# Performance work log

Hardware: AMD Instinct MI355X
Metric: run time of the kernel (lower is better)

The kernel has to match this reference:

```python
import jax, jax.numpy as jnp
import numpy as np

N_NODES = 65536
VOCAB = 1000
IN_DIM = 256
MEM_DIM = 256
HIDDEN = 256
NUM_CLASSES = 2


def _rand_parents(rng, n):
    # parent[i] < i for i >= 1 ; node 0 is the root (parent entry unused/masked)
    p = np.zeros(n, dtype=np.int64)
    p[1:] = rng.integers(0, np.arange(1, n))
    return jnp.asarray(p, dtype=jnp.int32)


def setup_inputs() -> dict:
    key = jax.random.key(0)
    ks = jax.random.split(key, 16)
    rng = np.random.default_rng(0)
    s = 0.05
    return {
        "l_tokens": jax.random.randint(ks[0], (N_NODES,), 0, VOCAB, dtype=jnp.int32),
        "l_parent": _rand_parents(rng, N_NODES),
        "r_tokens": jax.random.randint(ks[1], (N_NODES,), 0, VOCAB, dtype=jnp.int32),
        "r_parent": _rand_parents(rng, N_NODES),
        "emb_W": jax.random.normal(ks[2], (VOCAB, IN_DIM), jnp.float32) * s,
        "Wioux": jax.random.normal(ks[3], (IN_DIM, 3 * MEM_DIM), jnp.float32) * s,
        "bioux": jax.random.normal(ks[4], (3 * MEM_DIM,), jnp.float32) * s,
        "Wiouh": jax.random.normal(ks[5], (MEM_DIM, 3 * MEM_DIM), jnp.float32) * s,
        "biouh": jax.random.normal(ks[6], (3 * MEM_DIM,), jnp.float32) * s,
        "Wfx": jax.random.normal(ks[7], (IN_DIM, MEM_DIM), jnp.float32) * s,
        "bfx": jax.random.normal(ks[8], (MEM_DIM,), jnp.float32) * s,
        "Wfh": jax.random.normal(ks[9], (MEM_DIM, MEM_DIM), jnp.float32) * s,
        "bfh": jax.random.normal(ks[10], (MEM_DIM,), jnp.float32) * s,
        "Wh": jax.random.normal(ks[11], (2 * MEM_DIM, HIDDEN), jnp.float32) * s,
        "bh": jax.random.normal(ks[12], (HIDDEN,), jnp.float32) * s,
        "Wp": jax.random.normal(ks[13], (HIDDEN, NUM_CLASSES), jnp.float32) * s,
        "bp": jax.random.normal(ks[14], (NUM_CLASSES,), jnp.float32) * s,
    }


def _tree_lstm_root_c(tokens, parent, emb_W, Wioux, bioux, Wiouh, biouh,
                      Wfx, bfx, Wfh, bfh):
    # Batched x-dependent projections (faithful: ioux(emb), fx(emb))
    X = emb_W[tokens]                       # [N, in_dim]
    ioux_all = X @ Wioux + bioux            # [N, 3M]
    fx_all = X @ Wfx + bfx                  # [N, M]
    n = tokens.shape[0]
    m = Wfh.shape[0]

    def step(carry, i):
        h_sum, fc_sum, c_root = carry
        # ChildSumTreeLSTM.node_forward for node i
        iou = ioux_all[i] + h_sum[i] @ Wiouh + biouh
        ig, og, ug = jnp.split(iou, 3)
        c = jax.nn.sigmoid(ig) * jnp.tanh(ug) + fc_sum[i]   # leaf: fc_sum=0, h_sum=0
        h = jax.nn.sigmoid(og) * jnp.tanh(c)
        # forget-gate contribution of node i to its parent p:
        p = parent[i]
        f = jax.nn.sigmoid(h @ Wfh + bfh + fx_all[p])
        mask = (i != 0).astype(h.dtype)      # root has no parent
        h_sum = h_sum.at[p].add(h * mask)
        fc_sum = fc_sum.at[p].add(f * c * mask)
        c_root = jnp.where(i == 0, c, c_root)
        return (h_sum, fc_sum, c_root), None

    init = (jnp.zeros((n, m), X.dtype), jnp.zeros((n, m), X.dtype),
            jnp.zeros((m,), X.dtype))
    # children-before-parents order: descending index (parent[i] < i)
    (h_sum, fc_sum, c_root), _ = jax.lax.scan(step, init, jnp.arange(n - 1, -1, -1))
    return c_root                            # lstate == root cell state c


def reference(l_tokens, l_parent, r_tokens, r_parent, emb_W, Wioux, bioux,
              Wiouh, biouh, Wfx, bfx, Wfh, bfh, Wh, bh, Wp, bp):
    cl = _tree_lstm_root_c(l_tokens, l_parent, emb_W, Wioux, bioux, Wiouh,
                           biouh, Wfx, bfx, Wfh, bfh)
    cr = _tree_lstm_root_c(r_tokens, r_parent, emb_W, Wioux, bioux, Wiouh,
                           biouh, Wfx, bfx, Wfh, bfh)
    # Similarity head on root cell states
    vec = jnp.concatenate([cl * cr, jnp.abs(cl - cr)])[None, :]  # [1, 2M]
    hid = jax.nn.sigmoid(vec @ Wh + bh)
    return jax.nn.softmax(hid @ Wp + bp, axis=1)                 # [1, num_classes]
```

## Files before the change

### kernel.cpp

```cpp
#include <hip/hip_runtime.h>
#include <math.h>

#define NN 65536
#define TWO_N (2 * NN)
#define VOCAB 1000
#define MD 256
#define G3 768
#define DMAX 65536
#define HALF (DMAX / 2)
#define DCAP 128
#define NB 64
#define NT 256
#define NTS 1024
#define NSPAN 1024
#define SPAN 128
#define NTEAMS 64

typedef __attribute__((ext_vector_type(8))) short bf16x8;
typedef __attribute__((ext_vector_type(4))) float f32x4;

struct Params {
    const int* l_tokens; const int* l_parent;
    const int* r_tokens; const int* r_parent;
    const float* emb_W;
    const float* Wioux; const float* bioux;
    const float* Wiouh; const float* biouh;
    const float* Wfx;   const float* bfx;
    const float* Wfh;   const float* bfh;
    const float* Wh;    const float* bh;
    const float* Wp;    const float* bp;
    float* out;
    float* E_ioux;
    float* E_fx;
    float* C_leaf;
    float* H_leaf;
    float* FH_leaf;
    unsigned int* Wiouh_p;
    unsigned int* Wfh_p;
    float* h_sum;
    float* fc_sum;
    float* c_root;
    unsigned short* hstage;
    int* tarr;
    unsigned long long* ad_a;
    unsigned long long* ad_b;
    int* hc;
    int* pending;
    int* pend2;
    int* rank;
    int* lstart;
    int* blocksum;
    int* cnt; int* offs; int* cur;
    int* order;
    int* lorder;
    int* gtab;
    int* gdb;
    int* ecut;
    int* dbase;
    int* maxd;
    int cap_rows;
};

struct SWT {
    unsigned int wiou[12 * 2048];
    unsigned short hbufA[NB * MD];
    int nid[2][NB]; int row[2][NB]; int prow[2][NB];
    int tok[2][NB]; int ptok[2][NB]; int pgid[2][NB];
};

__device__ __forceinline__ float sigmoidf_(float x) {
    return 1.0f / (1.0f + __expf(-x));
}
__device__ __forceinline__ float tanhf_(float x) {
    float ex = __expf(2.0f * x);
    return 1.0f - 2.0f / (ex + 1.0f);
}
__device__ __forceinline__ unsigned int bf16rne_(float x) {
    unsigned int b = __float_as_uint(x);
    return (b + 0x7FFFu + ((b >> 16) & 1u)) >> 16;
}
__device__ __forceinline__ int aload_(int* p) {
    return __hip_atomic_load(p, __ATOMIC_RELAXED, __HIP_MEMORY_SCOPE_AGENT);
}
__device__ __forceinline__ float acohf_(const float* p) {
    return __hip_atomic_load((float*)p, __ATOMIC_RELAXED,
                             __HIP_MEMORY_SCOPE_AGENT);
}
__device__ __forceinline__ unsigned long long acohu64_(const void* p) {
    return __hip_atomic_load((unsigned long long*)p, __ATOMIC_RELAXED,
                             __HIP_MEMORY_SCOPE_AGENT);
}
__device__ __forceinline__ int dep_(const Params& P, int g) {
    return ((const int*)P.ad_a)[2 * g];
}
__device__ __forceinline__ int rowr(const Params& P, int tree, int d, int lr) {
    int r = P.dbase[tree * HALF + d] + lr;
    if (r >= P.cap_rows) r -= P.cap_rows;
    return r;
}

__global__ __launch_bounds__(NT) void k_prep(Params P) {
    __shared__ float es[4][MD];
    const int t = threadIdx.x, bid = blockIdx.x, nblk = gridDim.x;
    const int gsize = nblk * NT, gtid = bid * NT + t;
    for (int u = gtid; u < 48 * 2048; u += gsize) {
        int tl = u >> 11, rem = u & 2047;
        int kb = rem >> 8, rem2 = rem & 255;
        int ln = rem2 >> 2, jj = (rem2 & 3) << 1;
        int k = kb * 32 + (ln >> 4) * 8 + jj;
        int n = tl * 16 + (ln & 15);
        float x0 = P.Wiouh[(size_t)k * G3 + n];
        float x1 = P.Wiouh[(size_t)(k + 1) * G3 + n];
        P.Wiouh_p[u] = bf16rne_(x0) | (bf16rne_(x1) << 16);
    }
    for (int u = gtid; u < 16 * 2048; u += gsize) {
        int tl = u >> 11, rem = u & 2047;
        int kb = rem >> 8, rem2 = rem & 255;
        int ln = rem2 >> 2, jj = (rem2 & 3) << 1;
        int k = kb * 32 + (ln >> 4) * 8 + jj;
        int n = tl * 16 + (ln & 15);
        float x0 = P.Wfh[(size_t)k * MD + n];
        float x1 = P.Wfh[(size_t)(k + 1) * MD + n];
        P.Wfh_p[u] = bf16rne_(x0) | (bf16rne_(x1) << 16);
    }
    for (int v0 = bid * 4; v0 < VOCAB; v0 += nblk * 4) {
        __syncthreads();
        #pragma unroll
        for (int r = 0; r < 4; ++r)
            es[r][t] = (v0 + r < VOCAB) ? P.emb_W[(size_t)(v0 + r) * MD + t] : 0.f;
        __syncthreads();
        float a0[4] = {0.f,0.f,0.f,0.f}, a1[4] = {0.f,0.f,0.f,0.f};
        float a2[4] = {0.f,0.f,0.f,0.f}, a3[4] = {0.f,0.f,0.f,0.f};
        for (int k = 0; k < MD; ++k) {
            float wi = P.Wioux[k * G3 + t];
            float wo = P.Wioux[k * G3 + 256 + t];
            float wu = P.Wioux[k * G3 + 512 + t];
            float wf = P.Wfx[k * MD + t];
            #pragma unroll
            for (int r = 0; r < 4; ++r) {
                float e = es[r][k];
                a0[r] += wi * e; a1[r] += wo * e; a2[r] += wu * e; a3[r] += wf * e;
            }
        }
        float bi = P.bioux[t], bo = P.bioux[256 + t], bu = P.bioux[512 + t], bf = P.bfx[t];
        float hb_i = P.biouh[t], hb_o = P.biouh[256 + t], hb_u = P.biouh[512 + t];
        __syncthreads();
        for (int r = 0; r < 4; ++r) {
            float hl = 0.f;
            if (v0 + r < VOCAB) {
                float ei = a0[r] + bi, eo = a1[r] + bo, eu = a2[r] + bu;
                P.E_ioux[(size_t)(v0 + r) * G3 + t]       = ei;
                P.E_ioux[(size_t)(v0 + r) * G3 + 256 + t] = eo;
                P.E_ioux[(size_t)(v0 + r) * G3 + 512 + t] = eu;
                P.E_fx[(size_t)(v0 + r) * MD + t]         = a3[r] + bf;
                float cl = sigmoidf_(ei + hb_i) * tanhf_(eu + hb_u);
                hl = sigmoidf_(eo + hb_o) * tanhf_(cl);
                P.C_leaf[(size_t)(v0 + r) * MD + t] = cl;
                P.H_leaf[(size_t)(v0 + r) * MD + t] = hl;
            }
            es[r][t] = hl;
        }
        __syncthreads();
        float af[4] = {0.f,0.f,0.f,0.f};
        for (int k = 0; k < MD; ++k) {
            float wf = P.Wfh[(size_t)k * MD + t];
            #pragma unroll
            for (int r = 0; r < 4; ++r) af[r] += wf * es[r][k];
        }
        for (int r = 0; r < 4; ++r)
            if (v0 + r < VOCAB) P.FH_leaf[(size_t)(v0 + r) * MD + t] = af[r];
        __syncthreads();
    }
    for (int g = gtid; g < TWO_N; g += gsize) {
        int tree = g >> 16, i = g & (NN - 1);
        if (i == 0) {
            P.ad_a[g] = ((unsigned long long)g << 32);
        } else {
            const int* par = tree ? P.r_parent : P.l_parent;
            int pg = (tree << 16) | par[i];
            P.ad_a[g] = ((unsigned long long)pg << 32) | 1ull;
            P.hc[pg] = 1;
        }
    }
}

__global__ __launch_bounds__(NT) void k_double(Params P, int it) {
    const int gtid = blockIdx.x * NT + threadIdx.x;
    const int gsize = gridDim.x * NT;
    if (it == 0) {
        for (int g = gtid; g < TWO_N; g += gsize) {
            int i = g & (NN - 1);
            if (i != 0 && !P.hc[g]) {
                int tree = g >> 16;
                const int* par = tree ? P.r_parent : P.l_parent;
                atomicAdd(&P.pending[(tree << 16) | par[i]], 1);
            }
        }
    }
    unsigned long long* pa = (it & 1) ? P.ad_b : P.ad_a;
    unsigned long long* q  = (it & 1) ? P.ad_a : P.ad_b;
    for (int g = gtid; g < TWO_N; g += gsize) {
        if (!P.hc[g]) continue;
        unsigned long long v = pa[g];
        unsigned long long va = pa[v >> 32];
        q[g] = (va & 0xFFFFFFFF00000000ull)
             | (unsigned long long)((unsigned int)v + (unsigned int)va);
    }
}

__global__ __launch_bounds__(NT) void k_s1(Params P) {
    __shared__ int hcnt[2 * DCAP];
    __shared__ int hmax2[2];
    const int t = threadIdx.x, bid = blockIdx.x, nblk = gridDim.x;
    const int gsize = nblk * NT, gtid = bid * NT + t;
    for (int i = t; i < 2 * DCAP; i += NT) hcnt[i] = 0;
    if (t < 2) hmax2[t] = 0;
    __syncthreads();
    for (int g = gtid; g < TWO_N; g += gsize) {
        if (!P.hc[g]) continue;
        int tree = g >> 16;
        int d = dep_(P, g);
        if (d < DCAP) {
            atomicAdd(&hcnt[tree * DCAP + d], 1);
            atomicMax(&hmax2[tree], d);
        } else {
            atomicAdd(&P.cnt[tree * DMAX + d], 1);
            atomicMax(&P.maxd[tree], d);
        }
    }
    __syncthreads();
    for (int i = t; i < 2 * DCAP; i += NT) {
        int c = hcnt[i];
        if (c > 0) atomicAdd(&P.cnt[(i >= DCAP ? DMAX : 0) + (i & (DCAP - 1))], c);
    }
    if (t < 2) atomicMax(&P.maxd[t], hmax2[t]);
    for (int sp = bid; sp < NSPAN; sp += nblk) {
        __syncthreads();
        if (t < SPAN) hcnt[t] = P.pending[sp * SPAN + t];
        __syncthreads();
        for (int off = 1; off < SPAN; off <<= 1) {
            int a = (t >= off && t < SPAN) ? hcnt[t - off] : 0;
            __syncthreads();
            if (t < SPAN) hcnt[t] += a;
            __syncthreads();
        }
        if (t < SPAN) {
            int excl = t ? hcnt[t - 1] : 0;
            P.lstart[sp * SPAN + t] = excl;
        }
        if (t == SPAN - 1) P.blocksum[sp] = hcnt[t];
    }
}

__global__ __launch_bounds__(NT) void k_s2(Params P) {
    __shared__ int hcnt[NT];
    const int t = threadIdx.x;
    int4 v = ((const int4*)P.blocksum)[t];
    int s4 = v.x + v.y + v.z + v.w;
    hcnt[t] = s4;
    __syncthreads();
    for (int off = 1; off < NT; off <<= 1) {
        int a = (t >= off) ? hcnt[t - off] : 0;
        __syncthreads();
        hcnt[t] += a;
        __syncthreads();
    }
    int excl = t ? hcnt[t - 1] : 0;
    int4 r;
    r.x = excl; r.y = r.x + v.x; r.z = r.y + v.y; r.w = r.z + v.z;
    ((int4*)P.blocksum)[t] = r;
    if (t == NT - 1) P.maxd[23] = hcnt[NT - 1];
    __syncthreads();
    if (t < 2) {
        int tree = t;
        int run = tree * NN;
        int md = P.maxd[tree];
        for (int d = 0; d <= md; ++d) {
            P.offs[tree * DMAX + d] = run;
            run += P.cnt[tree * DMAX + d];
        }
    }
    __syncthreads();
    int md0 = P.maxd[0], md1 = P.maxd[1];
    int smax = md0 > md1 ? md0 : md1;
    if (t == 0) {
        long p = 0;
        for (int d = smax; d >= 0; --d) {
            P.dbase[d] = (int)(p % (long)P.cap_rows);
            p += P.cnt[d];
            P.dbase[HALF + d] = (int)(p % (long)P.cap_rows);
            p += P.cnt[DMAX + d];
        }
        int e = 0, hi = smax;
        while (hi >= 0) {
            long s = (long)(P.cnt[hi] + P.cnt[DMAX + hi]);
            if (hi > 0) s += P.cnt[hi - 1] + P.cnt[DMAX + hi - 1];
            int lo = hi;
            while (lo > 0) {
                long add = (lo - 1 > 0)
                    ? (P.cnt[lo - 2] + P.cnt[DMAX + lo - 2]) : 0;
                if (s + add > (long)P.cap_rows) break;
                s += add; --lo;
            }
            P.ecut[e++] = lo;
            hi = lo - 1;
        }
        P.maxd[24] = e;
        int j = 0;
        for (int d = smax; d >= 0; --d) {
            P.gdb[d] = j;
            j += (P.cnt[d] + NB - 1) / NB + (P.cnt[DMAX + d] + NB - 1) / NB;
        }
        P.maxd[22] = j;
    }
    __syncthreads();
    for (int d = t; d <= smax; d += NT) {
        int j = P.gdb[d];
        for (int tr = 0; tr < 2; ++tr) {
            int mdt = tr ? md1 : md0;
            int n = (d <= mdt) ? P.cnt[tr * DMAX + d] : 0;
            int st = P.offs[tr * DMAX + d];
            for (int b = 0; b < n; b += NB) {
                int cv = n - b; if (cv > NB) cv = NB;
                P.gtab[j++] = (st + b) | (cv << 20);
            }
        }
    }
}

__global__ __launch_bounds__(NT) void k_p2(Params P) {
    const int gtid = blockIdx.x * NT + threadIdx.x;
    const int gsize = gridDim.x * NT;
    for (int i = gtid; i < TWO_N; i += gsize)
        P.lstart[i] += P.blocksum[i >> 7];
}

__global__ __launch_bounds__(NT) void k_s3(Params P) {
    __shared__ int hcnt[2 * DCAP];
    __shared__ int hbase[2 * DCAP];
    const int t = threadIdx.x, bid = blockIdx.x, nblk = gridDim.x;
    const int gsize = nblk * NT, gtid = bid * NT + t;
    for (int i = t; i < 2 * DCAP; i += NT) hcnt[i] = 0;
    __syncthreads();
    for (int g = gtid; g < TWO_N; g += gsize) {
        if (!P.hc[g]) continue;
        int tree = g >> 16;
        int d = dep_(P, g);
        if (d < DCAP) atomicAdd(&hcnt[tree * DCAP + d], 1);
    }
    __syncthreads();
    for (int i = t; i < 2 * DCAP; i += NT) {
        int c = hcnt[i];
        if (c > 0) {
            int idx = (i >= DCAP ? DMAX : 0) + (i & (DCAP - 1));
            hbase[i] = P.offs[idx] + atomicAdd(&P.cur[idx], c);
        }
        hcnt[i] = 0;
    }
    __syncthreads();
    for (int g = gtid; g < TWO_N; g += gsize) {
        int tree = g >> 16, i = g & (NN - 1);
        if (P.hc[g]) {
            int d = dep_(P, g);
            if (d < DCAP) {
                int b = tree * DCAP + d;
                int pos = atomicAdd(&hcnt[b], 1);
                int gp = hbase[b] + pos;
                P.order[gp] = g;
                P.rank[g] = gp - P.offs[tree * DMAX + d];
            } else {
                int idx = tree * DMAX + d;
                int pos = atomicAdd(&P.cur[idx], 1);
                P.order[P.offs[idx] + pos] = g;
                P.rank[g] = pos;
            }
        } else if (i != 0) {
            const int* par = tree ? P.r_parent : P.l_parent;
            const int* toks = tree ? P.r_tokens : P.l_tokens;
            int pg = (tree << 16) | par[i];
            int pos = __hip_atomic_fetch_add(&P.pending[pg], -1,
                          __ATOMIC_RELAXED, __HIP_MEMORY_SCOPE_AGENT) - 1;
            P.lorder[P.lstart[pg] + pos] = toks[i];
        }
    }
}

__global__ __launch_bounds__(NT) void k_seed(Params P, int e) {
    const int t = threadIdx.x, bid = blockIdx.x, nblk = gridDim.x;
    int nep = P.maxd[24];
    if (e >= nep) return;
    int md0 = P.maxd[0], md1 = P.maxd[1];
    int smax = md0 > md1 ? md0 : md1;
    int hi = smax;
    for (int k = 0; k < e; ++k) hi = P.ecut[k] - 1;
    int lo = P.ecut[e];
    int sa = (lo > 0) ? lo - 1 : 0;
    int sb = (e == 0) ? hi : hi - 1;
    if (sa <= sb) {
        float b_f = P.bfh[t];
        for (int tree = 0; tree < 2; ++tree) {
            int mdt = tree ? md1 : md0;
            int bb = sb < mdt ? sb : mdt;
            if (sa > bb) continue;
            int st = P.offs[tree * DMAX + sa];
            int en = P.offs[tree * DMAX + bb] + P.cnt[tree * DMAX + bb];
            for (int idx = st + bid; idx < en; idx += nblk) {
                int g = P.order[idx];
                int i = g & (NN - 1);
                int tok = (tree ? P.r_tokens : P.l_tokens)[i];
                int d = dep_(P, g);
                int row = rowr(P, tree, d, P.rank[g]);
                int ls = P.lstart[g];
                int le = (g + 1 < TWO_N) ? P.lstart[g + 1] : P.maxd[23];
                float efx = P.E_fx[(size_t)tok * MD + t] + b_f;
                float ha = 0.f, fa = 0.f;
                for (int k = ls; k < le; ++k) {
                    int lt = P.lorder[k];
                    ha += P.H_leaf[(size_t)lt * MD + t];
                    fa += sigmoidf_(P.FH_leaf[(size_t)lt * MD + t] + efx)
                          * P.C_leaf[(size_t)lt * MD + t];
                }
                P.h_sum[(size_t)row * MD + t] = ha;
                P.fc_sum[(size_t)row * MD + t] = fa;
            }
        }
    }
    if (e == 0) {
        const int gsize = nblk * NT, gtid = bid * NT + t;
        for (int g = gtid; g < TWO_N; g += gsize) {
            int i = g & (NN - 1);
            if (i != 0 && P.hc[g]) {
                int tree = g >> 16;
                const int* par = tree ? P.r_parent : P.l_parent;
                int pg = (tree << 16) | par[i];
                atomicAdd(&P.pending[pg], 4);
                atomicAdd(&P.pend2[pg], 4);
            }
        }
    }
}

__device__ __forceinline__ void load_meta(const Params& P, SWT& sm, int jj,
                                          int buf, int t) {
    if (t < NB) {
        int g = -1, row = 0, prow = 0, tok = 0, ptok = 0, pgid = 0;
        int en = P.gtab[jj];
        int base = en & 0xFFFFF, cntv = en >> 20;
        if (t < cntv) {
            g = P.order[base + t];
            int tree = g >> 16, i = g & (NN - 1);
            const int* toks = tree ? P.r_tokens : P.l_tokens;
            const int* pars = tree ? P.r_parent : P.l_parent;
            tok = toks[i];
            int d = dep_(P, g);
            row = rowr(P, tree, d, P.rank[g]);
            if (i != 0) {
                int pl = pars[i];
                ptok = toks[pl];
                pgid = (tree << 16) | pl;
                prow = rowr(P, tree, d - 1, P.rank[pgid]);
            }
        }
        sm.nid[buf][t] = g; sm.row[buf][t] = row; sm.prow[buf][t] = prow;
        sm.tok[buf][t] = tok; sm.ptok[buf][t] = ptok; sm.pgid[buf][t] = pgid;
    }
}

__global__ __launch_bounds__(NTS, 1) void k_sweep(Params P, int e) {
    __shared__ SWT sm;
    int nep = P.maxd[24];
    if (e >= nep) return;
    const int t = threadIdx.x;
    const int b4 = blockIdx.x & 3;
    const int team = blockIdx.x >> 2;
    const int nteams = gridDim.x >> 2;
    const int wv = t >> 6;
    const int l = t & 63, lr = l >> 4, nloc = l & 15;

    for (int u = t; u < 12 * 2048; u += NTS) {
        int lt = u >> 11;
        int gate = lt >> 2, wq = lt & 3;
        sm.wiou[u] = P.Wiouh_p[(size_t)(gate * 16 + b4 * 4 + wq) * 2048 + (u & 2047)];
    }

    int md0 = P.maxd[0], md1 = P.maxd[1];
    int smax = md0 > md1 ? md0 : md1;
    int hi = smax;
    for (int k = 0; k < e; ++k) hi = P.ecut[k] - 1;
    int lo = P.ecut[e];
    int GT = P.maxd[22];
    int jend = (lo > 0) ? P.gdb[lo - 1] : GT;

    const unsigned short* Wl = (const unsigned short*)sm.wiou;
    const unsigned short* Wfg = (const unsigned short*)P.Wfh_p;
    int* tarr = P.tarr + e * NTEAMS + team;
    int kloc = 0;
    int cur = 0;

    const int j0 = P.gdb[hi] + team;
    if (j0 < jend) load_meta(P, sm, j0, 0, t);

    for (int j = j0; j < jend; j += nteams, ++kloc) {
        int en = P.gtab[j];
        int cntv = en >> 20;
        int nrb = (cntv + 15) >> 4;
        int ntask = nrb * 4;
        if (t < NB) {
            int g = sm.nid[cur][t];
            if (g >= 0) {
                while (aload_(&P.pending[g]) != 0) __builtin_amdgcn_s_sleep(4);
            }
        }
        __syncthreads();

        const int mtot2 = (nrb << 4) * (MD / 2);
        for (int u = t; u < mtot2; u += NTS) {
            int m = u >> 7, c2 = (u & 127) << 1;
            unsigned int pk = 0;
            if (sm.nid[cur][m] >= 0) {
                unsigned long long d2 =
                    acohu64_(&P.h_sum[(size_t)sm.row[cur][m] * MD + c2]);
                float v0 = __uint_as_float((unsigned int)d2);
                float v1 = __uint_as_float((unsigned int)(d2 >> 32));
                pk = bf16rne_(v0) | (bf16rne_(v1) << 16);
            }
            *(unsigned int*)&sm.hbufA[m * MD + (c2 ^ ((m & 7) << 3))] = pk;
        }
        __syncthreads();

        f32x4 aiv, aov, auv;
        float crg[4];
        const int tt = wv;
        const int rb = tt >> 2, q = tt & 3;
        const int n = (b4 * 4 + q) * 16 + nloc;
        const int tq = b4 * 4 + q;
        if (tt < ntask) {
            float b_i = P.biouh[n], b_o = P.biouh[256 + n], b_u = P.biouh[512 + n];
            #pragma unroll
            for (int r = 0; r < 4; ++r) {
                int m = rb * 16 + lr * 4 + r;
                float vi = 0.f, vo = 0.f, vu = 0.f;
                if (sm.nid[cur][m] >= 0) {
                    const float* Ei = P.E_ioux + (size_t)sm.tok[cur][m] * G3 + n;
                    vi = Ei[0] + b_i;
                    vo = Ei[256] + b_o;
                    vu = Ei[512] + b_u;
                }
                aiv[r] = vi; aov[r] = vo; auv[r] = vu;
            }
            #pragma unroll
            for (int kb = 0; kb < 8; ++kb) {
                int idx = (rb * 16 + nloc) * MD +
                          ((kb * 32 + lr * 8) ^ ((nloc & 7) << 3));
                bf16x8 afr = *(const bf16x8*)&sm.hbufA[idx];
                bf16x8 bi = *(const bf16x8*)&Wl[((q) * 8 + kb) * 512 + l * 8];
                bf16x8 bo = *(const bf16x8*)&Wl[((4 + q) * 8 + kb) * 512 + l * 8];
                bf16x8 bu = *(const bf16x8*)&Wl[((8 + q) * 8 + kb) * 512 + l * 8];
                aiv = __builtin_amdgcn_mfma_f32_16x16x32_bf16(afr, bi, aiv, 0, 0, 0);
                aov = __builtin_amdgcn_mfma_f32_16x16x32_bf16(afr, bo, aov, 0, 0, 0);
                auv = __builtin_amdgcn_mfma_f32_16x16x32_bf16(afr, bu, auv, 0, 0, 0);
            }
        }

        if (t < NB) {
            int g = sm.nid[cur][t];
            if (g >= 0) {
                while (aload_(&P.pend2[g]) != 0) __builtin_amdgcn_s_sleep(4);
            }
        }
        __syncthreads();

        unsigned short* hs = P.hstage
            + ((size_t)(team * 2 + (kloc & 1))) * (NB * MD);
        if (tt < ntask) {
            #pragma unroll
            for (int r = 0; r < 4; ++r) {
                int m = rb * 16 + lr * 4 + r;
                int g = sm.nid[cur][m];
                float c = 0.f, h = 0.f;
                if (g >= 0) {
                    float fcv = acohf_(&P.fc_sum[(size_t)sm.row[cur][m] * MD + n]);
                    c = sigmoidf_(aiv[r]) * tanhf_(auv[r]) + fcv;
                    h = sigmoidf_(aov[r]) * tanhf_(c);
                    int i = g & (NN - 1);
                    if (i == 0) {
                        P.c_root[(g >> 16) * MD + n] = c;
                    } else {
                        atomicAdd(&P.h_sum[(size_t)sm.prow[cur][m] * MD + n], h);
                    }
                }
                __hip_atomic_store(&hs[m * MD + n],
                                   (unsigned short)bf16rne_(h),
                                   __ATOMIC_RELAXED, __HIP_MEMORY_SCOPE_AGENT);
                crg[r] = c;
            }
        }

        __syncthreads();
        if (t < NB) {
            if (t == 0) {
                __hip_atomic_fetch_add(tarr, 1, __ATOMIC_RELAXED,
                                       __HIP_MEMORY_SCOPE_AGENT);
            }
            int g = sm.nid[cur][t];
            if (g >= 0 && (g & (NN - 1)) != 0) {
                __hip_atomic_fetch_add(&P.pending[sm.pgid[cur][t]], -1,
                                       __ATOMIC_RELAXED, __HIP_MEMORY_SCOPE_AGENT);
            }
        }
        if (j + nteams < jend) load_meta(P, sm, j + nteams, cur ^ 1, t);
        if (t == 0) {
            while (aload_(tarr) < 4 * (kloc + 1)) __builtin_amdgcn_s_sleep(2);
        }
        __syncthreads();

        const unsigned long long* hs64 = (const unsigned long long*)hs;
        if (tt < ntask) {
            float b_f = P.bfh[n];
            f32x4 af;
            #pragma unroll
            for (int r = 0; r < 4; ++r) {
                int m = rb * 16 + lr * 4 + r;
                int g = sm.nid[cur][m];
                float v = 0.f;
                if (g >= 0 && (g & (NN - 1)) != 0)
                    v = b_f + P.E_fx[(size_t)sm.ptok[cur][m] * MD + n];
                af[r] = v;
            }
            #pragma unroll
            for (int kb = 0; kb < 8; ++kb) {
                union { unsigned long long u[2]; bf16x8 v; } hu;
                int u0 = ((rb * 16 + nloc) * 128 + (kb * 32 + lr * 8) / 2) >> 1;
                hu.u[0] = acohu64_(&hs64[u0]);
                hu.u[1] = acohu64_(&hs64[u0 + 1]);
                bf16x8 bf = *(const bf16x8*)&Wfg[((tq * 8 + kb) * 64 + l) * 8];
                af = __builtin_amdgcn_mfma_f32_16x16x32_bf16(hu.v, bf, af, 0, 0, 0);
            }
            #pragma unroll
            for (int r = 0; r < 4; ++r) {
                int m = rb * 16 + lr * 4 + r;
                int g = sm.nid[cur][m];
                if (g >= 0 && (g & (NN - 1)) != 0) {
                    atomicAdd(&P.fc_sum[(size_t)sm.prow[cur][m] * MD + n],
                              sigmoidf_(af[r]) * crg[r]);
                }
            }
        }

        __syncthreads();
        if (t < NB) {
            int g = sm.nid[cur][t];
            if (g >= 0 && (g & (NN - 1)) != 0) {
                __hip_atomic_fetch_add(&P.pend2[sm.pgid[cur][t]], -1,
                                       __ATOMIC_RELAXED, __HIP_MEMORY_SCOPE_AGENT);
            }
        }
        cur ^= 1;
    }
}

__global__ __launch_bounds__(NT) void k_head(Params P) {
    __shared__ float vec[2 * MD];
    __shared__ float red[2][NT];
    const int t = threadIdx.x;
    float cl = P.c_root[t], cr = P.c_root[MD + t];
    vec[t] = cl * cr;
    vec[MD + t] = fabsf(cl - cr);
    __syncthreads();
    float acc = 0.f;
    for (int j = 0; j < 2 * MD; ++j) acc += vec[j] * P.Wh[(size_t)j * MD + t];
    float hid = sigmoidf_(acc + P.bh[t]);
    red[0][t] = hid * P.Wp[t * 2 + 0];
    red[1][t] = hid * P.Wp[t * 2 + 1];
    __syncthreads();
    for (int s = 128; s > 0; s >>= 1) {
        if (t < s) {
            red[0][t] += red[0][t + s];
            red[1][t] += red[1][t + s];
        }
        __syncthreads();
    }
    if (t == 0) {
        float l0 = red[0][0] + P.bp[0];
        float l1 = red[1][0] + P.bp[1];
        float mx = fmaxf(l0, l1);
        float e0 = __expf(l0 - mx), e1 = __expf(l1 - mx);
        float inv = 1.0f / (e0 + e1);
        P.out[0] = e0 * inv;
        P.out[1] = e1 * inv;
    }
}

extern "C" void kernel_launch(void* const* d_in, const int* in_sizes, int n_in,
                              void* d_out, int out_size, void* d_ws, size_t ws_size,
                              hipStream_t stream) {
    Params P;
    P.l_tokens = (const int*)d_in[0];
    P.l_parent = (const int*)d_in[1];
    P.r_tokens = (const int*)d_in[2];
    P.r_parent = (const int*)d_in[3];
    P.emb_W = (const float*)d_in[4];
    P.Wioux = (const float*)d_in[5];
    P.bioux = (const float*)d_in[6];
    P.Wiouh = (const float*)d_in[7];
    P.biouh = (const float*)d_in[8];
    P.Wfx   = (const float*)d_in[9];
    P.bfx   = (const float*)d_in[10];
    P.Wfh   = (const float*)d_in[11];
    P.bfh   = (const float*)d_in[12];
    P.Wh    = (const float*)d_in[13];
    P.bh    = (const float*)d_in[14];
    P.Wp    = (const float*)d_in[15];
    P.bp    = (const float*)d_in[16];
    P.out   = (float*)d_out;

    char* w = (char*)d_ws;
    auto alloc = [&](size_t bytes) {
        char* r = w;
        w += (bytes + 255) & ~(size_t)255;
        return r;
    };
    P.E_ioux   = (float*)alloc((size_t)VOCAB * G3 * 4);
    P.E_fx     = (float*)alloc((size_t)VOCAB * MD * 4);
    P.C_leaf   = (float*)alloc((size_t)VOCAB * MD * 4);
    P.H_leaf   = (float*)alloc((size_t)VOCAB * MD * 4);
    P.FH_leaf  = (float*)alloc((size_t)VOCAB * MD * 4);
    P.Wiouh_p  = (unsigned int*)alloc((size_t)48 * 2048 * 4);
    P.Wfh_p    = (unsigned int*)alloc((size_t)16 * 2048 * 4);
    P.c_root   = (float*)alloc(2 * MD * 4);
    P.hstage   = (unsigned short*)alloc((size_t)NTEAMS * 2 * NB * MD * 2);
    P.tarr     = (int*)alloc((size_t)8 * NTEAMS * 4);
    P.ad_a     = (unsigned long long*)alloc((size_t)TWO_N * 8);
    P.ad_b     = (unsigned long long*)alloc((size_t)TWO_N * 8);
    P.hc       = (int*)alloc((size_t)TWO_N * 4);
    P.pending  = (int*)alloc((size_t)TWO_N * 4);
    P.pend2    = (int*)alloc((size_t)TWO_N * 4);
    P.cnt      = (int*)alloc((size_t)2 * DMAX * 4);
    P.offs     = (int*)alloc((size_t)2 * DMAX * 4);
    P.cur      = (int*)alloc((size_t)2 * DMAX * 4);
    P.order    = (int*)alloc((size_t)TWO_N * 4);
    P.rank     = (int*)alloc((size_t)TWO_N * 4);
    P.lstart   = (int*)alloc((size_t)TWO_N * 4);
    P.lorder   = (int*)alloc((size_t)TWO_N * 4);
    P.blocksum = (int*)alloc((size_t)NSPAN * 4);
    P.gtab     = (int*)alloc((size_t)(TWO_N / 16 + 2 * DMAX + 256) * 4);
    P.gdb      = (int*)alloc((size_t)DMAX * 4);
    P.ecut     = (int*)alloc((size_t)DMAX * 4);
    P.dbase    = (int*)alloc((size_t)DMAX * 4);
    P.maxd     = (int*)alloc(256);

    size_t used = (size_t)(w - (char*)d_ws);
    size_t remain = (ws_size > used) ? (ws_size - used) : 0;
    size_t cap = remain / ((size_t)2 * MD * 4);
    if (cap > (size_t)TWO_N) cap = TWO_N;
    P.cap_rows = (int)cap;
    P.h_sum  = (float*)w;
    P.fc_sum = P.h_sum + cap * MD;

    hipMemsetAsync(P.hc, 0, (size_t)3 * TWO_N * 4, stream);
    hipMemsetAsync(P.cnt, 0, (size_t)3 * 2 * DMAX * 4, stream);
    hipMemsetAsync(P.maxd, 0, 256, stream);
    hipMemsetAsync(P.tarr, 0, (size_t)8 * NTEAMS * 4, stream);

    k_prep<<<dim3(512), dim3(NT), 0, stream>>>(P);
    for (int it = 0; it < 6; ++it)
        k_double<<<dim3(512), dim3(NT), 0, stream>>>(P, it);
    k_s1<<<dim3(NSPAN), dim3(NT), 0, stream>>>(P);
    k_s2<<<dim3(1), dim3(NT), 0, stream>>>(P);
    k_p2<<<dim3(512), dim3(NT), 0, stream>>>(P);
    k_s3<<<dim3(NSPAN), dim3(NT), 0, stream>>>(P);

    for (int e = 0; e < 6; ++e) {
        k_seed<<<dim3(1024), dim3(NT), 0, stream>>>(P, e);
        k_sweep<<<dim3(4 * NTEAMS), dim3(NTS), 0, stream>>>(P, e);
    }
    k_head<<<dim3(1), dim3(NT), 0, stream>>>(P);
}
```

Before: 911.4 us.

## Process sparse deep tree levels in a dedicated single-block-per-tree tail kernel

Adds a k_tail kernel with one 1024-thread block per tree. It walks the deepest levels, where each tree has at most 64 nodes per level, synchronising with __syncthreads instead of the multi-team sweep's cross-block signalling. The sweep for epoch 0 then starts below that depth cutoff (D0). The aim is to cut the per-level synchronisation latency across the long, narrow deep part of random trees, at the cost of running those levels with only two workgroups. The tail path runs only when there is a single epoch (maxd[24]==1), and D0 is computed only when e==1.

```diff
diff --git a/kernel.cpp b/kernel.cpp
--- a/kernel.cpp
+++ b/kernel.cpp
@@ -68,6 +68,13 @@
     int tok[2][NB]; int ptok[2][NB]; int pgid[2][NB];
 };
 
+struct SWTAIL {
+    unsigned short hbufA[NB * MD];
+    unsigned short hbufB[NB * MD];
+    int nid[NB]; int row[NB]; int prow[NB]; int tok[NB]; int ptok[NB];
+    int pgid[NB];
+};
+
 __device__ __forceinline__ float sigmoidf_(float x) {
     return 1.0f / (1.0f + __expf(-x));
 }
@@ -312,6 +319,13 @@
             j += (P.cnt[d] + NB - 1) / NB + (P.cnt[DMAX + d] + NB - 1) / NB;
         }
         P.maxd[22] = j;
+        int D0 = smax + 1;
+        if (e == 1) {
+            int dd = smax;
+            while (dd >= 1 && P.cnt[dd] <= 64 && P.cnt[DMAX + dd] <= 64) --dd;
+            D0 = dd + 1;
+        }
+        P.maxd[25] = D0;
     }
     __syncthreads();
     for (int d = t; d <= smax; d += NT) {
@@ -440,6 +454,160 @@
     }
 }
 
+__global__ __launch_bounds__(NTS, 1) void k_tail(Params P) {
+    __shared__ SWTAIL sm;
+    if (P.maxd[24] != 1) return;
+    const int tree = blockIdx.x;
+    const int D0 = P.maxd[25];
+    const int md = P.maxd[tree];
+    if (D0 > md) return;
+    const int t = threadIdx.x;
+    const int wv = t >> 6;
+    const int l = t & 63, lr = l >> 4, nloc = l & 15;
+    const int tq = wv;
+    const int n = tq * 16 + nloc;
+    const unsigned short* Wg = (const unsigned short*)P.Wiouh_p;
+    const unsigned short* Wfg = (const unsigned short*)P.Wfh_p;
+    const float b_i = P.biouh[n], b_o = P.biouh[256 + n], b_u = P.biouh[512 + n];
+    const float b_f = P.bfh[n];
+    const int* toks = tree ? P.r_tokens : P.l_tokens;
+    const int* pars = tree ? P.r_parent : P.l_parent;
+
+    for (int d = md; d >= D0; --d) {
+        const int n0 = P.cnt[tree * DMAX + d];
+        if (n0 == 0) continue;
+        const int base = P.offs[tree * DMAX + d];
+        const int nrb = (n0 + 15) >> 4;
+        __syncthreads();
+        if (t < NB) {
+            int g = -1, row = 0, prow = 0, tok = 0, ptok = 0, pgid = 0;
+            if (t < n0) {
+                g = P.order[base + t];
+                int i = g & (NN - 1);
+                tok = toks[i];
+                row = rowr(P, tree, d, P.rank[g]);
+                if (i != 0) {
+                    int pl = pars[i];
+                    ptok = toks[pl];
+                    pgid = (tree << 16) | pl;
+                    prow = rowr(P, tree, d - 1, P.rank[pgid]);
+                }
+            }
+            sm.nid[t] = g; sm.row[t] = row; sm.prow[t] = prow;
+            sm.tok[t] = tok; sm.ptok[t] = ptok; sm.pgid[t] = pgid;
+        }
+        __syncthreads();
+        const int mtot2 = (nrb << 4) * (MD / 2);
+        for (int u = t; u < mtot2; u += NTS) {
+            int m = u >> 7, c2 = (u & 127) << 1;
+            unsigned int pk = 0;
+            if (sm.nid[m] >= 0) {
+                unsigned long long d2 =
+                    acohu64_(&P.h_sum[(size_t)sm.row[m] * MD + c2]);
+                float v0 = __uint_as_float((unsigned int)d2);
+                float v1 = __uint_as_float((unsigned int)(d2 >> 32));
+                pk = bf16rne_(v0) | (bf16rne_(v1) << 16);
+            }
+            *(unsigned int*)&sm.hbufA[m * MD + (c2 ^ ((m & 7) << 3))] = pk;
+        }
+        __syncthreads();
+        float crg[4][4];
+        #pragma unroll
+        for (int rb = 0; rb < 4; ++rb) {
+            if (rb < nrb) {
+                f32x4 aiv, aov, auv;
+                #pragma unroll
+                for (int r = 0; r < 4; ++r) {
+                    int m = rb * 16 + lr * 4 + r;
+                    float vi = 0.f, vo = 0.f, vu = 0.f;
+                    if (sm.nid[m] >= 0) {
+                        const float* Ei = P.E_ioux + (size_t)sm.tok[m] * G3 + n;
+                        vi = Ei[0] + b_i;
+                        vo = Ei[256] + b_o;
+                        vu = Ei[512] + b_u;
+                    }
+                    aiv[r] = vi; aov[r] = vo; auv[r] = vu;
+                }
+                #pragma unroll
+                for (int kb = 0; kb < 8; ++kb) {
+                    int idx = (rb * 16 + nloc) * MD +
+                              ((kb * 32 + lr * 8) ^ ((nloc & 7) << 3));
+                    bf16x8 afr = *(const bf16x8*)&sm.hbufA[idx];
+                    bf16x8 bi = *(const bf16x8*)&Wg[(((tq) * 8 + kb) * 64 + l) * 8];
+                    bf16x8 bo = *(const bf16x8*)&Wg[(((16 + tq) * 8 + kb) * 64 + l) * 8];
+                    bf16x8 bu = *(const bf16x8*)&Wg[(((32 + tq) * 8 + kb) * 64 + l) * 8];
+                    aiv = __builtin_amdgcn_mfma_f32_16x16x32_bf16(afr, bi, aiv, 0, 0, 0);
+                    aov = __builtin_amdgcn_mfma_f32_16x16x32_bf16(afr, bo, aov, 0, 0, 0);
+                    auv = __builtin_amdgcn_mfma_f32_16x16x32_bf16(afr, bu, auv, 0, 0, 0);
+                }
+                #pragma unroll
+                for (int r = 0; r < 4; ++r) {
+                    int m = rb * 16 + lr * 4 + r;
+                    int g = sm.nid[m];
+                    float c = 0.f, h = 0.f;
+                    if (g >= 0) {
+                        float fcv = acohf_(&P.fc_sum[(size_t)sm.row[m] * MD + n]);
+                        c = sigmoidf_(aiv[r]) * tanhf_(auv[r]) + fcv;
+                        h = sigmoidf_(aov[r]) * tanhf_(c);
+                        int i = g & (NN - 1);
+                        if (i == 0) {
+                            P.c_root[tree * MD + n] = c;
+                        } else {
+                            atomicAdd(&P.h_sum[(size_t)sm.prow[m] * MD + n], h);
+                        }
+                    }
+                    sm.hbufB[m * MD + (n ^ ((m & 7) << 3))] =
+                        (unsigned short)bf16rne_(h);
+                    crg[rb][r] = c;
+                }
+            }
+        }
+        __syncthreads();
+        #pragma unroll
+        for (int rb = 0; rb < 4; ++rb) {
+            if (rb < nrb) {
+                f32x4 af;
+                #pragma unroll
+                for (int r = 0; r < 4; ++r) {
+                    int m = rb * 16 + lr * 4 + r;
+                    int g = sm.nid[m];
+                    float v = 0.f;
+                    if (g >= 0 && (g & (NN - 1)) != 0)
+                        v = b_f + P.E_fx[(size_t)sm.ptok[m] * MD + n];
+                    af[r] = v;
+                }
+                #pragma unroll
+                for (int kb = 0; kb < 8; ++kb) {
+                    int idx = (rb * 16 + nloc) * MD +
+                              ((kb * 32 + lr * 8) ^ ((nloc & 7) << 3));
+                    bf16x8 afr = *(const bf16x8*)&sm.hbufB[idx];
+                    bf16x8 bf = *(const bf16x8*)&Wfg[((tq * 8 + kb) * 64 + l) * 8];
+                    af = __builtin_amdgcn_mfma_f32_16x16x32_bf16(afr, bf, af, 0, 0, 0);
+                }
+                #pragma unroll
+                for (int r = 0; r < 4; ++r) {
+                    int m = rb * 16 + lr * 4 + r;
+                    int g = sm.nid[m];
+                    if (g >= 0 && (g & (NN - 1)) != 0) {
+                        atomicAdd(&P.fc_sum[(size_t)sm.prow[m] * MD + n],
+                                  sigmoidf_(af[r]) * crg[rb][r]);
+                    }
+                }
+            }
+        }
+        __syncthreads();
+        if (t < NB) {
+            int g = sm.nid[t];
+            if (g >= 0 && (g & (NN - 1)) != 0) {
+                __hip_atomic_fetch_add(&P.pending[sm.pgid[t]], -4,
+                                       __ATOMIC_RELAXED, __HIP_MEMORY_SCOPE_AGENT);
+                __hip_atomic_fetch_add(&P.pend2[sm.pgid[t]], -4,
+                                       __ATOMIC_RELAXED, __HIP_MEMORY_SCOPE_AGENT);
+            }
+        }
+    }
+}
+
 __device__ __forceinline__ void load_meta(const Params& P, SWT& sm, int jj,
                                           int buf, int t) {
     if (t < NB) {
@@ -488,6 +656,10 @@
     int hi = smax;
     for (int k = 0; k < e; ++k) hi = P.ecut[k] - 1;
     int lo = P.ecut[e];
+    if (e == 0) {
+        int D0 = P.maxd[25];
+        if (D0 - 1 < hi) hi = D0 - 1;
+    }
     int GT = P.maxd[22];
     int jend = (lo > 0) ? P.gdb[lo - 1] : GT;
 
@@ -770,7 +942,10 @@
     k_p2<<<dim3(512), dim3(NT), 0, stream>>>(P);
     k_s3<<<dim3(NSPAN), dim3(NT), 0, stream>>>(P);
 
-    for (int e = 0; e < 6; ++e) {
+    k_seed<<<dim3(1024), dim3(NT), 0, stream>>>(P, 0);
+    k_tail<<<dim3(2), dim3(NTS), 0, stream>>>(P);
+    k_sweep<<<dim3(4 * NTEAMS), dim3(NTS), 0, stream>>>(P, 0);
+    for (int e = 1; e < 6; ++e) {
         k_seed<<<dim3(1024), dim3(NT), 0, stream>>>(P, e);
         k_sweep<<<dim3(4 * NTEAMS), dim3(NTS), 0, stream>>>(P, e);
     }
```

Measured after the change: 997.7 us. 1.09x slower.
